# Kernel optimization log

Measured on AMD Instinct MI355X. Metric: run time of the kernel, lower is better.

Reference implementation:

```python
import jax, jax.numpy as jnp
import numpy as np

D_H = 1024

def _binary_operator(e_i, e_j):
    a_i, kv_i = e_i
    a_j, kv_j = e_j
    return (a_j * a_i, a_j * kv_i + kv_j)

def setup_inputs() -> dict:
    key = jax.random.key(0)
    k1, k2 = jax.random.split(key)
    B, S, D = 4, 4096, 1024
    x = jax.random.normal(k1, (B, S, D), dtype=jnp.float32)
    # nn.Dense default lecun_normal-ish scale; plain scaled normal is fine for a reference
    W = jax.random.normal(k2, (D, 3 * D_H), dtype=jnp.float32) * (1.0 / np.sqrt(D))
    b = jnp.zeros((3 * D_H,), dtype=jnp.float32)
    return {"x": x, "W": W, "b": b}

def reference(x, W, b):
    # projection: (B,S,D) @ (D, 3*d_h)
    proj = jnp.einsum('bsd,dh->bsh', x, W) + b
    inp = jnp.tanh(proj[:, :, :D_H])                 # (B,S,d_h)
    gates = jax.nn.sigmoid(proj[:, :, D_H:])         # (B,S,2*d_h)
    input_gate, output_gate = jnp.split(gates, 2, axis=-1)
    forget_gate = 1.0 - input_gate                   # tied gates
    _, hidden = jax.lax.associative_scan(
        _binary_operator, (forget_gate, inp * input_gate), axis=1)
    return jnp.tanh(hidden) * output_gate            # (B,S,d_h)
```

## Files before the change

### kernel.cpp

```cpp
#include <hip/hip_runtime.h>
#include <hip/hip_bf16.h>
#include <cmath>

typedef _Float16 half8 __attribute__((ext_vector_type(8)));
typedef _Float16 half4 __attribute__((ext_vector_type(4)));
typedef float f32x4 __attribute__((ext_vector_type(4)));

#define M_DIM 16384
#define K_DIM 1024
#define N_DIM 3072
#define S_LEN 4096
#define NCHUNK 64
#define CLEN 64

#define BM 256
#define BN 128
#define BK 64
#define NT 16
#define A_E 16384
#define SLOT_E 24576

__device__ __forceinline__ float sigmoid_f(float x) {
    return 1.0f / (1.0f + __expf(-x));
}

__global__ void k_cast_x(const float* __restrict__ x, _Float16* __restrict__ xb) {
    int i = blockIdx.x * blockDim.x + threadIdx.x;
    float4 v = reinterpret_cast<const float4*>(x)[i];
    half4 h;
    h.x = (_Float16)v.x; h.y = (_Float16)v.y;
    h.z = (_Float16)v.z; h.w = (_Float16)v.w;
    reinterpret_cast<half4*>(xb)[i] = h;
}

__global__ void k_cast_w(const float* __restrict__ W, _Float16* __restrict__ Wt) {
    __shared__ float t[64][65];
    const int k0 = (blockIdx.x / 48) * 64;
    const int n0 = (blockIdx.x % 48) * 64;
    const int c  = threadIdx.x & 63;
    const int r0 = threadIdx.x >> 6;
    #pragma unroll
    for (int i = 0; i < 16; ++i) {
        int r = r0 + i * 4;
        t[r][c] = W[(size_t)(k0 + r) * N_DIM + n0 + c];
    }
    __syncthreads();
    #pragma unroll
    for (int i = 0; i < 16; ++i) {
        int r = r0 + i * 4;
        Wt[(size_t)(n0 + r) * K_DIM + k0 + c] = (_Float16)t[c][r];
    }
}

__global__ __launch_bounds__(512, 2) void k_gemm(
    const _Float16* __restrict__ A,
    const _Float16* __restrict__ Bt,
    const float* __restrict__ bias,
    _Float16* __restrict__ G)
{
    extern __shared__ _Float16 lds[];

    const int tid  = threadIdx.x;
    const int lane = tid & 63;
    const int wid  = tid >> 6;
    const int wr   = wid >> 1;
    const int wc   = wid & 1;

    const int bid   = blockIdx.x;
    const int wg    = (bid & 7) * 192 + (bid >> 3);
    const int tileM = (wg / 24) * BM;
    const int tileN = (wg % 24) * BN;

    const int l3   = lane >> 3;
    const int c8   = lane & 7;
    const int scol = ((c8 ^ l3) << 3);
    const _Float16* gA = A  + (size_t)(tileM + wid * 8 + l3) * K_DIM + scol;
    const _Float16* gB = Bt + (size_t)(tileN + wid * 8 + l3) * K_DIM + scol;

    const int l15 = lane & 15;
    const int hi  = lane >> 4;
    const int swz = (l15 & 7) << 3;
    const int o0  = (hi * 8)      ^ swz;
    const int o1  = (32 + hi * 8) ^ swz;

    f32x4 acc[4][4] = {};

#define GL(SRC, DST) __builtin_amdgcn_global_load_lds( \
        (const __attribute__((address_space(1))) void*)(SRC), \
        (__attribute__((address_space(3))) void*)(DST), 16, 0, 0)

#define STAGE(kt, slot) do { \
        _Float16* as_ = lds + (slot) * SLOT_E + wid * 512; \
        _Float16* bs_ = lds + (slot) * SLOT_E + A_E + wid * 512; \
        const _Float16* ga_ = gA + (size_t)(kt) * BK; \
        const _Float16* gb_ = gB + (size_t)(kt) * BK; \
        GL(ga_,                        as_);          \
        GL(ga_ +  64 * K_DIM,          as_ + 4096);   \
        GL(ga_ + 128 * K_DIM,          as_ + 8192);   \
        GL(ga_ + 192 * K_DIM,          as_ + 12288);  \
        GL(gb_,                        bs_);          \
        GL(gb_ +  64 * K_DIM,          bs_ + 4096);   \
    } while (0)

    STAGE(0, 0);
    STAGE(1, 1);
    asm volatile("s_waitcnt vmcnt(6)" ::: "memory");
    __builtin_amdgcn_s_barrier();

    int sC = 0, sS = 2;
    #pragma unroll 1
    for (int t = 0; t < NT; ++t) {
        if (t + 2 < NT) STAGE(t + 2, sS);

        const _Float16* as = lds + sC * SLOT_E + (wr * 64 + l15) * 64;
        const _Float16* bs = lds + sC * SLOT_E + A_E + (wc * 64 + l15) * 64;
        half8 a0[4], a1[4], b0[4], b1[4];
        #pragma unroll
        for (int i = 0; i < 4; ++i) {
            a0[i] = *(const half8*)(as + i * 1024 + o0);
            a1[i] = *(const half8*)(as + i * 1024 + o1);
            b0[i] = *(const half8*)(bs + i * 1024 + o0);
            b1[i] = *(const half8*)(bs + i * 1024 + o1);
        }

        __builtin_amdgcn_s_setprio(1);
        #pragma unroll
        for (int i = 0; i < 4; ++i)
            #pragma unroll
            for (int j = 0; j < 4; ++j) {
                acc[i][j] = __builtin_amdgcn_mfma_f32_16x16x32_f16(a0[i], b0[j], acc[i][j], 0, 0, 0);
                acc[i][j] = __builtin_amdgcn_mfma_f32_16x16x32_f16(a1[i], b1[j], acc[i][j], 0, 0, 0);
            }
        __builtin_amdgcn_s_setprio(0);

        if (t < NT - 2)       asm volatile("s_waitcnt vmcnt(6)" ::: "memory");
        else if (t == NT - 2) asm volatile("s_waitcnt vmcnt(0)" ::: "memory");
        if (t < NT - 1) __builtin_amdgcn_s_barrier();

        if (++sC == 3) sC = 0;
        if (++sS == 3) sS = 0;
    }
#undef STAGE
#undef GL

    #pragma unroll
    for (int j = 0; j < 4; ++j) {
        const int n = tileN + wc * 64 + j * 16 + l15;
        const float bn = bias[n];
        const bool is_tanh = (n < 1024);
        #pragma unroll
        for (int i = 0; i < 4; ++i) {
            const int mb = tileM + wr * 64 + i * 16 + hi * 4;
            #pragma unroll
            for (int r = 0; r < 4; ++r) {
                float v = acc[i][j][r] + bn;
                G[(size_t)(mb + r) * N_DIM + n] = (_Float16)(is_tanh ? tanhf(v) : sigmoid_f(v));
            }
        }
    }
}

__global__ void k_scan1(const _Float16* __restrict__ G,
                        float* __restrict__ sumA, float* __restrict__ sumH) {
    const int gid   = blockIdx.x;
    const int dblk  = gid & 3;
    const int chunk = (gid >> 2) & 63;
    const int b     = gid >> 8;
    const int d     = dblk * 256 + threadIdx.x;

    const _Float16* base = G + (size_t)(b * S_LEN + chunk * CLEN) * N_DIM;
    float A = 1.0f, H = 0.0f;
    #pragma unroll 4
    for (int s = 0; s < CLEN; ++s) {
        float g0 = (float)base[(size_t)s * N_DIM + d];
        float g1 = (float)base[(size_t)s * N_DIM + 1024 + d];
        float a  = 1.0f - g1;
        float kv = g0 * g1;
        H = fmaf(a, H, kv);
        A *= a;
    }
    const int cidx = (b * NCHUNK + chunk) * 1024 + d;
    sumA[cidx] = A;
    sumH[cidx] = H;
}

__global__ void k_scan2(const float* __restrict__ sumA, const float* __restrict__ sumH,
                        float* __restrict__ pref) {
    const int c = blockIdx.x * blockDim.x + threadIdx.x;
    const int b = c >> 10;
    const int d = c & 1023;
    float h = 0.0f;
    #pragma unroll 8
    for (int chunk = 0; chunk < NCHUNK; ++chunk) {
        const int idx = (b * NCHUNK + chunk) * 1024 + d;
        pref[idx] = h;
        h = fmaf(sumA[idx], h, sumH[idx]);
    }
}

__global__ void k_scan3(const _Float16* __restrict__ G,
                        const float* __restrict__ pref,
                        float* __restrict__ out) {
    const int gid   = blockIdx.x;
    const int dblk  = gid & 3;
    const int chunk = (gid >> 2) & 63;
    const int b     = gid >> 8;
    const int d     = dblk * 256 + threadIdx.x;

    const _Float16* base = G + (size_t)(b * S_LEN + chunk * CLEN) * N_DIM;
    float h = pref[(b * NCHUNK + chunk) * 1024 + d];
    #pragma unroll 4
    for (int s = 0; s < CLEN; ++s) {
        float g0 = (float)base[(size_t)s * N_DIM + d];
        float g1 = (float)base[(size_t)s * N_DIM + 1024 + d];
        float g2 = (float)base[(size_t)s * N_DIM + 2048 + d];
        float a  = 1.0f - g1;
        float kv = g0 * g1;
        h = fmaf(a, h, kv);
        out[(size_t)(b * S_LEN + chunk * CLEN + s) * 1024 + d] = tanhf(h) * g2;
    }
}

extern "C" void kernel_launch(void* const* d_in, const int* in_sizes, int n_in,
                              void* d_out, int out_size, void* d_ws, size_t ws_size,
                              hipStream_t stream) {
    const float* x = (const float*)d_in[0];
    const float* W = (const float*)d_in[1];
    const float* b = (const float*)d_in[2];
    float* out = (float*)d_out;

    char* ws = (char*)d_ws;
    _Float16* xb = (_Float16*)ws;
    _Float16* Wt = (_Float16*)(ws + 33554432);
    _Float16* G  = (_Float16*)(ws + 33554432 + 6291456);
    float* sumA  = (float*)(ws + 140509184);
    float* sumH  = sumA + 4096 * NCHUNK;
    float* pref  = sumH + 4096 * NCHUNK;

    k_cast_x<<<16384, 256, 0, stream>>>(x, xb);
    k_cast_w<<<768,   256, 0, stream>>>(W, Wt);
    k_gemm <<<1536, 512, 3 * SLOT_E * sizeof(_Float16), stream>>>(xb, Wt, b, G);
    k_scan1<<<1024, 256, 0, stream>>>(G, sumA, sumH);
    k_scan2<<<16,   256, 0, stream>>>(sumA, sumH, pref);
    k_scan3<<<1024, 256, 0, stream>>>(G, pref, out);
    (void)in_sizes; (void)n_in; (void)out_size; (void)ws_size;
}
```

Measured before the change: 230.6 us.

## Enlarge GEMM tile to 256x256 with 8-phase ping-pong LDS pipeline

Switches the projection GEMM from 256x128 tiles with a triple-buffered stage loop to 256x256 tiles, where each wave computes a 128x64 sub-tile, over a double-buffered LDS. The K loop is split into eight phases, each loading one quarter of the next stage while MFMAs run on a quarter of the current fragments, with barriers between phases. This halves the block count and raises arithmetic intensity per LDS byte. In exchange it doubles the accumulator registers, uses 128KB of LDS so only one block fits per CU despite launch bounds of 2, and adds many barriers.

```diff
diff --git a/kernel.cpp b/kernel.cpp
--- a/kernel.cpp
+++ b/kernel.cpp
@@ -13,12 +13,8 @@
 #define NCHUNK 64
 #define CLEN 64
 
-#define BM 256
-#define BN 128
-#define BK 64
-#define NT 16
-#define A_E 16384
-#define SLOT_E 24576
+#define BUF_E 32768
+#define B_OFF 16384
 
 __device__ __forceinline__ float sigmoid_f(float x) {
     return 1.0f / (1.0f + __expf(-x));
@@ -63,84 +59,117 @@
     const int tid  = threadIdx.x;
     const int lane = tid & 63;
     const int wid  = tid >> 6;
-    const int wr   = wid >> 1;
-    const int wc   = wid & 1;
+    const int wr   = wid >> 2;
+    const int wc   = wid & 3;
 
     const int bid   = blockIdx.x;
-    const int wg    = (bid & 7) * 192 + (bid >> 3);
-    const int tileM = (wg / 24) * BM;
-    const int tileN = (wg % 24) * BN;
+    const int wg    = (bid & 7) * 96 + (bid >> 3);
+    const int tileM = (wg / 12) * 256;
+    const int tileN = (wg % 12) * 256;
 
     const int l3   = lane >> 3;
     const int c8   = lane & 7;
     const int scol = ((c8 ^ l3) << 3);
     const _Float16* gA = A  + (size_t)(tileM + wid * 8 + l3) * K_DIM + scol;
     const _Float16* gB = Bt + (size_t)(tileN + wid * 8 + l3) * K_DIM + scol;
+    _Float16* const sA = lds + wid * 512;
+    _Float16* const sB = lds + B_OFF + wid * 512;
 
     const int l15 = lane & 15;
     const int hi  = lane >> 4;
     const int swz = (l15 & 7) << 3;
     const int o0  = (hi * 8)      ^ swz;
     const int o1  = (32 + hi * 8) ^ swz;
-
-    f32x4 acc[4][4] = {};
+    const _Float16* arow = lds + (wr * 128 + l15) * 64;
+    const _Float16* brow = lds + B_OFF + (wc * 64 + l15) * 64;
+
+    f32x4 acc[8][4] = {};
+    half8 a[4][2], b[4][2];
 
 #define GL(SRC, DST) __builtin_amdgcn_global_load_lds( \
         (const __attribute__((address_space(1))) void*)(SRC), \
         (__attribute__((address_space(3))) void*)(DST), 16, 0, 0)
 
-#define STAGE(kt, slot) do { \
-        _Float16* as_ = lds + (slot) * SLOT_E + wid * 512; \
-        _Float16* bs_ = lds + (slot) * SLOT_E + A_E + wid * 512; \
-        const _Float16* ga_ = gA + (size_t)(kt) * BK; \
-        const _Float16* gb_ = gB + (size_t)(kt) * BK; \
-        GL(ga_,                        as_);          \
-        GL(ga_ +  64 * K_DIM,          as_ + 4096);   \
-        GL(ga_ + 128 * K_DIM,          as_ + 8192);   \
-        GL(ga_ + 192 * K_DIM,          as_ + 12288);  \
-        GL(gb_,                        bs_);          \
-        GL(gb_ +  64 * K_DIM,          bs_ + 4096);   \
-    } while (0)
-
-    STAGE(0, 0);
-    STAGE(1, 1);
-    asm volatile("s_waitcnt vmcnt(6)" ::: "memory");
-    __builtin_amdgcn_s_barrier();
-
-    int sC = 0, sS = 2;
+#define STAGE_A(kt, half, bufe) do { \
+        const _Float16* g_ = gA + (size_t)(kt) * 64 + (size_t)((half) * 128) * K_DIM; \
+        GL(g_,                       sA + (bufe) + (half) * 8192);        \
+        GL(g_ + (size_t)64 * K_DIM,  sA + (bufe) + (half) * 8192 + 4096); \
+    } while (0)
+
+#define STAGE_B(kt, half, bufe) do { \
+        const _Float16* g_ = gB + (size_t)(kt) * 64 + (size_t)((half) * 128) * K_DIM; \
+        GL(g_,                       sB + (bufe) + (half) * 8192);        \
+        GL(g_ + (size_t)64 * K_DIM,  sB + (bufe) + (half) * 8192 + 4096); \
+    } while (0)
+
+#define RD_A(bufe, mh) do { const _Float16* p_ = arow + (bufe) + (mh) * 4096; \
+        a[0][0] = *(const half8*)(p_ + o0);        a[0][1] = *(const half8*)(p_ + o1); \
+        a[1][0] = *(const half8*)(p_ + 1024 + o0); a[1][1] = *(const half8*)(p_ + 1024 + o1); \
+        a[2][0] = *(const half8*)(p_ + 2048 + o0); a[2][1] = *(const half8*)(p_ + 2048 + o1); \
+        a[3][0] = *(const half8*)(p_ + 3072 + o0); a[3][1] = *(const half8*)(p_ + 3072 + o1); \
+    } while (0)
+
+#define RD_B(bufe, nh) do { const _Float16* p_ = brow + (bufe) + (nh) * 2048; \
+        b[(nh)*2+0][0] = *(const half8*)(p_ + o0);        b[(nh)*2+0][1] = *(const half8*)(p_ + o1); \
+        b[(nh)*2+1][0] = *(const half8*)(p_ + 1024 + o0); b[(nh)*2+1][1] = *(const half8*)(p_ + 1024 + o1); \
+    } while (0)
+
+#define MFMA_Q(mh, nh) do { \
+        __builtin_amdgcn_s_setprio(1); \
+        _Pragma("unroll") \
+        for (int m_ = 0; m_ < 4; ++m_) { \
+            _Pragma("unroll") \
+            for (int n_ = 0; n_ < 2; ++n_) { \
+                acc[(mh)*4+m_][(nh)*2+n_] = __builtin_amdgcn_mfma_f32_16x16x32_f16( \
+                    a[m_][0], b[(nh)*2+n_][0], acc[(mh)*4+m_][(nh)*2+n_], 0, 0, 0); \
+                acc[(mh)*4+m_][(nh)*2+n_] = __builtin_amdgcn_mfma_f32_16x16x32_f16( \
+                    a[m_][1], b[(nh)*2+n_][1], acc[(mh)*4+m_][(nh)*2+n_], 0, 0, 0); \
+            } } \
+        __builtin_amdgcn_s_setprio(0); \
+    } while (0)
+
+#define BAR() do { __builtin_amdgcn_s_barrier(); asm volatile("" ::: "memory"); } while (0)
+#define VM4() asm volatile("s_waitcnt vmcnt(4)" ::: "memory")
+#define VM0() asm volatile("s_waitcnt vmcnt(0)" ::: "memory")
+
+    STAGE_B(0, 0, 0); STAGE_B(0, 1, 0);
+    STAGE_A(0, 0, 0); STAGE_A(0, 1, 0);
+    STAGE_B(1, 0, BUF_E); STAGE_A(1, 0, BUF_E);
+    VM4();
+    BAR();
+
     #pragma unroll 1
-    for (int t = 0; t < NT; ++t) {
-        if (t + 2 < NT) STAGE(t + 2, sS);
-
-        const _Float16* as = lds + sC * SLOT_E + (wr * 64 + l15) * 64;
-        const _Float16* bs = lds + sC * SLOT_E + A_E + (wc * 64 + l15) * 64;
-        half8 a0[4], a1[4], b0[4], b1[4];
-        #pragma unroll
-        for (int i = 0; i < 4; ++i) {
-            a0[i] = *(const half8*)(as + i * 1024 + o0);
-            a1[i] = *(const half8*)(as + i * 1024 + o1);
-            b0[i] = *(const half8*)(bs + i * 1024 + o0);
-            b1[i] = *(const half8*)(bs + i * 1024 + o1);
-        }
-
-        __builtin_amdgcn_s_setprio(1);
-        #pragma unroll
-        for (int i = 0; i < 4; ++i)
-            #pragma unroll
-            for (int j = 0; j < 4; ++j) {
-                acc[i][j] = __builtin_amdgcn_mfma_f32_16x16x32_f16(a0[i], b0[j], acc[i][j], 0, 0, 0);
-                acc[i][j] = __builtin_amdgcn_mfma_f32_16x16x32_f16(a1[i], b1[j], acc[i][j], 0, 0, 0);
-            }
-        __builtin_amdgcn_s_setprio(0);
-
-        if (t < NT - 2)       asm volatile("s_waitcnt vmcnt(6)" ::: "memory");
-        else if (t == NT - 2) asm volatile("s_waitcnt vmcnt(0)" ::: "memory");
-        if (t < NT - 1) __builtin_amdgcn_s_barrier();
-
-        if (++sC == 3) sC = 0;
-        if (++sS == 3) sS = 0;
-    }
-#undef STAGE
+    for (int it = 0; it < 8; ++it) {
+        const int kt0 = 2 * it;
+        RD_A(0, 0); RD_B(0, 0);
+        STAGE_B(kt0 + 1, 1, BUF_E);
+        BAR(); MFMA_Q(0, 0); BAR();
+        RD_B(0, 1);
+        STAGE_A(kt0 + 1, 1, BUF_E);
+        BAR(); MFMA_Q(0, 1); BAR();
+        RD_A(0, 1);
+        if (it < 7) STAGE_B(kt0 + 2, 0, 0);
+        BAR(); MFMA_Q(1, 0); BAR();
+        if (it < 7) { STAGE_B(kt0 + 2, 1, 0); VM4(); } else { VM0(); }
+        BAR(); MFMA_Q(1, 1); BAR();
+        RD_A(BUF_E, 0); RD_B(BUF_E, 0);
+        if (it < 7) STAGE_A(kt0 + 2, 0, 0);
+        BAR(); MFMA_Q(0, 0); BAR();
+        RD_B(BUF_E, 1);
+        if (it < 7) STAGE_A(kt0 + 2, 1, 0);
+        BAR(); MFMA_Q(0, 1); BAR();
+        RD_A(BUF_E, 1);
+        if (it < 7) STAGE_B(kt0 + 3, 0, BUF_E);
+        BAR(); MFMA_Q(1, 0); BAR();
+        if (it < 7) { STAGE_A(kt0 + 3, 0, BUF_E); VM4(); }
+        BAR(); MFMA_Q(1, 1); BAR();
+    }
+
+#undef STAGE_A
+#undef STAGE_B
+#undef RD_A
+#undef RD_B
+#undef MFMA_Q
 #undef GL
 
     #pragma unroll
@@ -149,8 +178,8 @@
         const float bn = bias[n];
         const bool is_tanh = (n < 1024);
         #pragma unroll
-        for (int i = 0; i < 4; ++i) {
-            const int mb = tileM + wr * 64 + i * 16 + hi * 4;
+        for (int i = 0; i < 8; ++i) {
+            const int mb = tileM + wr * 128 + i * 16 + hi * 4;
             #pragma unroll
             for (int r = 0; r < 4; ++r) {
                 float v = acc[i][j][r] + bn;
@@ -239,7 +268,7 @@
 
     k_cast_x<<<16384, 256, 0, stream>>>(x, xb);
     k_cast_w<<<768,   256, 0, stream>>>(W, Wt);
-    k_gemm <<<1536, 512, 3 * SLOT_E * sizeof(_Float16), stream>>>(xb, Wt, b, G);
+    k_gemm <<<768, 512, 131072, stream>>>(xb, Wt, b, G);
     k_scan1<<<1024, 256, 0, stream>>>(G, sumA, sumH);
     k_scan2<<<16,   256, 0, stream>>>(sumA, sumH, pref);
     k_scan3<<<1024, 256, 0, stream>>>(G, pref, out);
```

Result: faster. 219.4 us (-4.9%).
